# Optimization experiments

Hardware: AMD Instinct MI355X
Metric: run time of the kernel (lower is better)

## Reference

```python
import jax, jax.numpy as jnp
import numpy as np

B, T, C = 2, 2048, 1024
N_HEADS = 16
HEAD_DIM = C // N_HEADS

def setup_inputs() -> dict:
    key = jax.random.key(0)
    k1, k2, k3 = jax.random.split(key, 3)
    x = jax.random.normal(k1, (B, T, C), dtype=jnp.float32)
    W_qkv = jax.random.normal(k2, (C, 3 * C), dtype=jnp.float32) * (1.0 / np.sqrt(C))
    W_out = jax.random.normal(k3, (C, C), dtype=jnp.float32) * (1.0 / np.sqrt(C))
    return {"x": x, "W_qkv": W_qkv, "W_out": W_out}

def reference(x, W_qkv, W_out):
    b, t, c = x.shape
    qkv = jnp.einsum('btc,cd->btd', x, W_qkv)  # [B,T,3C]
    q, k, v = jnp.split(qkv, 3, axis=-1)
    # [B, H, T, hd]
    q = q.reshape(b, t, N_HEADS, HEAD_DIM).transpose(0, 2, 1, 3)
    k = k.reshape(b, t, N_HEADS, HEAD_DIM).transpose(0, 2, 1, 3)
    v = v.reshape(b, t, N_HEADS, HEAD_DIM).transpose(0, 2, 1, 3)
    scale = 1.0 / jnp.sqrt(jnp.asarray(HEAD_DIM, dtype=x.dtype))
    attn = jnp.einsum('bhqd,bhkd->bhqk', q, k) * scale  # [B,H,T,T]
    causal = jnp.tril(jnp.ones((t, t), dtype=bool))
    attn = jnp.where(causal, attn, jnp.asarray(-1e9, dtype=attn.dtype))
    attn = jax.nn.softmax(attn, axis=-1)
    out = jnp.einsum('bhqk,bhkd->bhqd', attn, v)
    out = out.transpose(0, 2, 1, 3).reshape(b, t, c)
    return jnp.einsum('btc,cd->btd', out, W_out)
```

## Files before the change

### kernel.cpp

```cpp
#include <hip/hip_runtime.h>
#include <hip/hip_bf16.h>

typedef __attribute__((ext_vector_type(8))) short short8;
typedef __attribute__((ext_vector_type(4))) short bf16x4;
typedef __attribute__((ext_vector_type(4))) float floatx4;

#define T_SEQ 2048
#define NH    16
#define HD    64
#define QSCALE 0.18033688f

#define MFMA16(a, b, c) __builtin_amdgcn_mfma_f32_16x16x16bf16_1k(a, b, c, 0, 0, 0)
#define MFMA32(a, b, c) __builtin_amdgcn_mfma_f32_16x16x32_bf16(a, b, c, 0, 0, 0)

__device__ __forceinline__ ushort f2bf(float f) {
    union { float f; unsigned u; } un; un.f = f;
    unsigned r = un.u + 0x7fff + ((un.u >> 16) & 1);
    return (ushort)(r >> 16);
}
__device__ __forceinline__ unsigned pkbf(float a, float b) {
    __hip_bfloat162 t = __float22bfloat162_rn(float2{a, b});
    return *reinterpret_cast<unsigned*>(&t);
}

typedef const __attribute__((address_space(1))) unsigned int* gp1_t;
typedef __attribute__((address_space(3))) unsigned int* lp3_t;
__device__ __forceinline__ void gl_lds16(const ushort* g, ushort* l) {
    __builtin_amdgcn_global_load_lds((gp1_t)g, (lp3_t)l, 16, 0, 0);
}

__global__ void prep_kernel(const float* __restrict__ Wqkv, const float* __restrict__ Wout,
                            const float* __restrict__ x, ushort* __restrict__ wt_qkv,
                            ushort* __restrict__ wt_out, ushort* __restrict__ x_bf) {
    __shared__ ushort tile[32][33];
    const int bid = blockIdx.x;
    if (bid >= 4096) {
        size_t i = ((size_t)(bid - 4096) * 256 + threadIdx.x) * 8;
        float4 f0 = *(const float4*)(x + i);
        float4 f1 = *(const float4*)(x + i + 4);
        short8 v;
        v[0] = (short)f2bf(f0.x); v[1] = (short)f2bf(f0.y);
        v[2] = (short)f2bf(f0.z); v[3] = (short)f2bf(f0.w);
        v[4] = (short)f2bf(f1.x); v[5] = (short)f2bf(f1.y);
        v[6] = (short)f2bf(f1.z); v[7] = (short)f2bf(f1.w);
        *(short8*)(x_bf + i) = v;
        return;
    }
    const float* in; ushort* out; int R, C, gx, gy;
    if (bid < 3072) { in = Wqkv; out = wt_qkv; R = 1024; C = 3072; gx = bid % 96; gy = bid / 96; }
    else            { int t = bid - 3072; in = Wout; out = wt_out; R = 1024; C = 1024; gx = t & 31; gy = t >> 5; }
    const int tx = threadIdx.x & 31, ty = threadIdx.x >> 5;
    const int bx = gx * 32, by = gy * 32;
    #pragma unroll
    for (int i = ty; i < 32; i += 8)
        tile[i][tx] = f2bf(in[(size_t)(by + i) * C + bx + tx]);
    __syncthreads();
    #pragma unroll
    for (int i = ty; i < 32; i += 8)
        out[(size_t)(bx + i) * R + by + tx] = tile[tx][i];
}

template <int EPI>
__global__ __launch_bounds__(256, 2)
void gemm_bt(const ushort* __restrict__ A, const ushort* __restrict__ Bt,
             void* __restrict__ O0, ushort* __restrict__ O1, ushort* __restrict__ O2,
             int M, int N, int K) {
    __shared__ __align__(16) ushort smem[8704];
    ushort* As = smem;
    ushort* Bs = smem + 4096;
    const int tid  = threadIdx.x;
    const int wave = tid >> 6, lane = tid & 63;
    const int quad = lane >> 4, l16 = lane & 15;
    const int wm = (wave >> 1) * 64, wn = (wave & 1) * 64;
    const int m0 = blockIdx.x * 128, n0 = blockIdx.y * 128;

    const int c0 = tid, c1 = tid + 256;
    const int row0 = c0 >> 2, row1 = c1 >> 2;
    const int g0 = (((c0 & 3) ^ ((row0 >> 1) & 3))) * 8;
    const int g1 = (((c1 & 3) ^ ((row1 >> 1) & 3))) * 8;
    const ushort* aP0 = A  + (size_t)(m0 + row0) * K + g0;
    const ushort* aP1 = A  + (size_t)(m0 + row1) * K + g1;
    const ushort* bP0 = Bt + (size_t)(n0 + row0) * K + g0;
    const ushort* bP1 = Bt + (size_t)(n0 + row1) * K + g1;

    floatx4 acc[4][4];
    #pragma unroll
    for (int i = 0; i < 4; i++)
        #pragma unroll
        for (int j = 0; j < 4; j++)
            acc[i][j] = (floatx4){0.f, 0.f, 0.f, 0.f};

    const int col_sw = (quad ^ ((l16 >> 1) & 3)) * 8;

    for (int k0 = 0; k0 < K; k0 += 32) {
        __syncthreads();
        gl_lds16(aP0 + k0, &As[c0 * 8]);
        gl_lds16(aP1 + k0, &As[c1 * 8]);
        gl_lds16(bP0 + k0, &Bs[c0 * 8]);
        gl_lds16(bP1 + k0, &Bs[c1 * 8]);
        __syncthreads();
        short8 af[4], bf[4];
        #pragma unroll
        for (int i = 0; i < 4; i++)
            af[i] = *(const short8*)(&As[(wm + i * 16 + l16) * 32 + col_sw]);
        #pragma unroll
        for (int j = 0; j < 4; j++)
            bf[j] = *(const short8*)(&Bs[(wn + j * 16 + l16) * 32 + col_sw]);
        #pragma unroll
        for (int i = 0; i < 4; i++)
            #pragma unroll
            for (int j = 0; j < 4; j++)
                acc[i][j] = __builtin_amdgcn_mfma_f32_16x16x32_bf16(af[i], bf[j], acc[i][j], 0, 0, 0);
    }

    if (EPI == 0 && n0 >= 2048) {
        const int b = m0 >> 11;
        const int t0 = m0 & 2047;
        const int head0 = (n0 - 2048) >> 6;
        __syncthreads();
        #pragma unroll
        for (int nh = 0; nh < 2; nh++) {
            if ((wave & 1) == nh) {
                #pragma unroll
                for (int j = 0; j < 4; j++)
                    #pragma unroll
                    for (int i = 0; i < 4; i++) {
                        int nl = j * 16 + l16;
                        int mB = wm + i * 16 + quad * 4;
                        *(unsigned*)(&smem[nl * 136 + mB])     = pkbf(acc[i][j][0], acc[i][j][1]);
                        *(unsigned*)(&smem[nl * 136 + mB + 2]) = pkbf(acc[i][j][2], acc[i][j][3]);
                    }
            }
            __syncthreads();
            #pragma unroll
            for (int cc = 0; cc < 4; cc++) {
                int c = cc * 256 + tid;
                int row = c >> 4, mcol = (c & 15) * 8;
                uint4 v = *(const uint4*)(&smem[row * 136 + mcol]);
                *(uint4*)(&O2[((size_t)(b * NH + head0 + nh) * HD + row) * T_SEQ + t0 + mcol]) = v;
            }
            __syncthreads();
        }
        return;
    }

    #pragma unroll
    for (int i = 0; i < 4; i++) {
        #pragma unroll
        for (int j = 0; j < 4; j++) {
            #pragma unroll
            for (int r = 0; r < 4; r++) {
                int m = m0 + wm + i * 16 + quad * 4 + r;
                int n = n0 + wn + j * 16 + l16;
                if (EPI == 0) {
                    int b = m >> 11, t = m & 2047;
                    int part = n >> 10, c = n & 1023;
                    int head = c >> 6, off = c & 63;
                    float av = acc[i][j][r];
                    if (part == 0) av *= QSCALE;
                    ushort v = f2bf(av);
                    if (part == 0) ((ushort*)O0)[(((size_t)(b * NH + head)) * T_SEQ + t) * HD + off] = v;
                    else           O1[(((size_t)(b * NH + head)) * T_SEQ + t) * HD + off] = v;
                } else {
                    ((float*)O0)[(size_t)m * N + n] = acc[i][j][r];
                }
            }
        }
    }
}

__device__ __forceinline__ void softmax_step(floatx4 s[4], float& mst, float& lst,
                                             floatx4 o[4], bf16x4 pf[4]) {
    float t0 = fmaxf(fmaxf(s[0][0], s[0][1]), fmaxf(s[0][2], s[0][3]));
    float t1 = fmaxf(fmaxf(s[1][0], s[1][1]), fmaxf(s[1][2], s[1][3]));
    float t2 = fmaxf(fmaxf(s[2][0], s[2][1]), fmaxf(s[2][2], s[2][3]));
    float t3 = fmaxf(fmaxf(s[3][0], s[3][1]), fmaxf(s[3][2], s[3][3]));
    float t = fmaxf(fmaxf(t0, t1), fmaxf(t2, t3));
    t = fmaxf(t, __shfl_xor(t, 16));
    t = fmaxf(t, __shfl_xor(t, 32));
    if (!__all(t - mst <= 8.0f)) {
        float mnew  = fmaxf(mst, t);
        float alpha = exp2f(mst - mnew);
        mst = mnew;
        lst *= alpha;
        #pragma unroll
        for (int db = 0; db < 4; db++)
            #pragma unroll
            for (int r = 0; r < 4; r++) o[db][r] *= alpha;
    }
    float lsum = 0.f;
    #pragma unroll
    for (int j = 0; j < 4; j++) {
        float p0 = exp2f(s[j][0] - mst);
        float p1 = exp2f(s[j][1] - mst);
        float p2 = exp2f(s[j][2] - mst);
        float p3 = exp2f(s[j][3] - mst);
        lsum += (p0 + p1) + (p2 + p3);
        union { bf16x4 v; unsigned u[2]; } pu;
        pu.u[0] = pkbf(p0, p1);
        pu.u[1] = pkbf(p2, p3);
        pf[j] = pu.v;
    }
    lsum += __shfl_xor(lsum, 16);
    lsum += __shfl_xor(lsum, 32);
    lst += lsum;
}

__global__ __launch_bounds__(256, 2)
void attn_kernel(const ushort* __restrict__ Q, const ushort* __restrict__ Kk,
                 const ushort* __restrict__ Vt, ushort* __restrict__ Oout) {
    __shared__ __align__(16) ushort Ks[2][64 * 64];
    __shared__ __align__(16) ushort Vs[2][64 * 64];
    const int tid  = threadIdx.x;
    const int wave = tid >> 6, lane = tid & 63;
    const int quad = lane >> 4, l16 = lane & 15;
    const int idx = blockIdx.x;
    const int bh = idx & 31;
    const int jp = idx >> 5;
    const int p  = (jp < 8) ? jp : (15 - (jp - 8));
    const int qtA = p, qtB = 31 - p;
    const int b = bh >> 4, h = bh & 15;

    const ushort* qp = Q  + (size_t)bh * T_SEQ * HD;
    const ushort* kp = Kk + (size_t)bh * T_SEQ * HD;
    const ushort* vp = Vt + (size_t)bh * HD * T_SEQ;

    const int q0A = qtA * 64 + wave * 16;
    const int q0B = qtB * 64 + wave * 16;

    short8 qfA[2], qfB[2];
    #pragma unroll
    for (int kb = 0; kb < 2; kb++) {
        qfA[kb] = *(const short8*)(qp + (size_t)(q0A + l16) * HD + kb * 32 + quad * 8);
        qfB[kb] = *(const short8*)(qp + (size_t)(q0B + l16) * HD + kb * 32 + quad * 8);
    }

    floatx4 oA[4], oB[4];
    #pragma unroll
    for (int db = 0; db < 4; db++) {
        oA[db] = (floatx4){0.f, 0.f, 0.f, 0.f};
        oB[db] = (floatx4){0.f, 0.f, 0.f, 0.f};
    }
    float mA = -1e30f, lA = 0.f, mB = -1e30f, lB = 0.f;

    const int c0 = tid, c1 = tid + 256;
    const int r0 = c0 >> 3, r1 = c1 >> 3;
    const int g0 = ((c0 & 7) ^ (r0 & 7)) * 8;
    const int g1 = ((c1 & 7) ^ (r1 & 7)) * 8;
    const size_t koff0 = (size_t)r0 * HD + g0,     koff1 = (size_t)r1 * HD + g1;
    const size_t voff0 = (size_t)r0 * T_SEQ + g0,  voff1 = (size_t)r1 * T_SEQ + g1;

    gl_lds16(kp + koff0, &Ks[0][c0 * 8]);
    gl_lds16(kp + koff1, &Ks[0][c1 * 8]);
    gl_lds16(vp + voff0, &Vs[0][c0 * 8]);
    gl_lds16(vp + voff1, &Vs[0][c1 * 8]);

    const int xsw = (l16 & 7), qh = quad >> 1, ql = quad & 1;
    const int ka0 = l16 * 64 + ((quad ^ xsw) * 8);
    const int ka1 = l16 * 64 + (((4 + quad) ^ xsw) * 8);
    int va[4];
    #pragma unroll
    for (int jj = 0; jj < 4; jj++)
        va[jj] = l16 * 64 + (((2 * jj + qh) ^ xsw) * 8) + ql * 4;

#define ATT_STEP(BUF, KT)                                                        \
    {                                                                            \
        __syncthreads();                                                         \
        if ((KT) < qtB) {                                                        \
            const size_t kbase = (size_t)((KT) + 1) * 64 * HD;                   \
            const int    vbase = ((KT) + 1) * 64;                                \
            gl_lds16(kp + kbase + koff0, &Ks[(BUF) ^ 1][c0 * 8]);                \
            gl_lds16(kp + kbase + koff1, &Ks[(BUF) ^ 1][c1 * 8]);                \
            gl_lds16(vp + vbase + voff0, &Vs[(BUF) ^ 1][c0 * 8]);                \
            gl_lds16(vp + vbase + voff1, &Vs[(BUF) ^ 1][c1 * 8]);                \
        }                                                                        \
        if ((KT) <= qtA) {                                                       \
                                \
            floatx4 sA[4], sB[4];                                                \
            _Pragma("unroll")                                                    \
            for (int jj = 0; jj < 4; jj++) {                                     \
                sA[jj] = (floatx4){0.f, 0.f, 0.f, 0.f};                          \
                sB[jj] = (floatx4){0.f, 0.f, 0.f, 0.f};                          \
            }                                                                    \
            __builtin_amdgcn_s_setprio(1);                                       \
            _Pragma("unroll")                                                    \
            for (int jj = 0; jj < 4; jj++) {                                     \
                short8 kf0 = *(const short8*)(&Ks[BUF][ka0 + jj * 1024]);        \
                sB[jj] = MFMA32(kf0, qfB[0], sB[jj]);                            \
                sA[jj] = MFMA32(kf0, qfA[0], sA[jj]);                            \
            }                                                                    \
            _Pragma("unroll")                                                    \
            for (int jj = 0; jj < 4; jj++) {                                     \
                short8 kf1 = *(const short8*)(&Ks[BUF][ka1 + jj * 1024]);        \
                sB[jj] = MFMA32(kf1, qfB[1], sB[jj]);                            \
                sA[jj] = MFMA32(kf1, qfA[1], sA[jj]);                            \
            }                                                                    \
            __builtin_amdgcn_s_setprio(0);                                       \
            if ((KT) == qtA) {                                                   \
                _Pragma("unroll")                                                \
                for (int jj = 0; jj < 4; jj++)                                   \
                    _Pragma("unroll")                                            \
                    for (int rr = 0; rr < 4; rr++)                               \
                        if (jj * 16 + quad * 4 + rr > wave * 16 + l16)           \
                            sA[jj][rr] = -1e30f;                                 \
            }                                                                    \
            bf16x4 pfA[4], pfB[4];                                               \
            softmax_step(sB, mB, lB, oB, pfB);                                   \
            softmax_step(sA, mA, lA, oA, pfA);                                   \
            __builtin_amdgcn_s_setprio(1);                                       \
            _Pragma("unroll")                                                    \
            for (int jj = 0; jj < 4; jj++)                                       \
                _Pragma("unroll")                                                \
                for (int db = 0; db < 4; db++) {                                 \
                    bf16x4 vf = *(const bf16x4*)(&Vs[BUF][va[jj] + db * 1024]);  \
                    oB[db] = MFMA16(vf, pfB[jj], oB[db]);                        \
                    oA[db] = MFMA16(vf, pfA[jj], oA[db]);                        \
                }                                                                \
            __builtin_amdgcn_s_setprio(0);                                       \
        } else {                                                                 \
                                                  \
            floatx4 sB[4];                                                       \
            _Pragma("unroll")                                                    \
            for (int jj = 0; jj < 4; jj++) sB[jj] = (floatx4){0.f, 0.f, 0.f, 0.f}; \
            __builtin_amdgcn_s_setprio(1);                                       \
            _Pragma("unroll")                                                    \
            for (int jj = 0; jj < 4; jj++) {                                     \
                short8 kf0 = *(const short8*)(&Ks[BUF][ka0 + jj * 1024]);        \
                sB[jj] = MFMA32(kf0, qfB[0], sB[jj]);                            \
            }                                                                    \
            _Pragma("unroll")                                                    \
            for (int jj = 0; jj < 4; jj++) {                                     \
                short8 kf1 = *(const short8*)(&Ks[BUF][ka1 + jj * 1024]);        \
                sB[jj] = MFMA32(kf1, qfB[1], sB[jj]);                            \
            }                                                                    \
            __builtin_amdgcn_s_setprio(0);                                       \
            if ((KT) == qtB) {                                                   \
                _Pragma("unroll")                                                \
                for (int jj = 0; jj < 4; jj++)                                   \
                    _Pragma("unroll")                                            \
                    for (int rr = 0; rr < 4; rr++)                               \
                        if (jj * 16 + quad * 4 + rr > wave * 16 + l16)           \
                            sB[jj][rr] = -1e30f;                                 \
            }                                                                    \
            bf16x4 pfB[4];                                                       \
            softmax_step(sB, mB, lB, oB, pfB);                                   \
            __builtin_amdgcn_s_setprio(1);                                       \
            _Pragma("unroll")                                                    \
            for (int jj = 0; jj < 4; jj++)                                       \
                _Pragma("unroll")                                                \
                for (int db = 0; db < 4; db++) {                                 \
                    bf16x4 vf = *(const bf16x4*)(&Vs[BUF][va[jj] + db * 1024]);  \
                    oB[db] = MFMA16(vf, pfB[jj], oB[db]);                        \
                }                                                                \
            __builtin_amdgcn_s_setprio(0);                                       \
        }                                                                        \
    }

    int kt = 0;
    for (; kt + 1 <= qtB; kt += 2) {
        ATT_STEP(0, kt)
        ATT_STEP(1, kt + 1)
    }
    if (kt <= qtB) ATT_STEP(0, kt)
#undef ATT_STEP

    {
        const float inv = 1.0f / lB;
        const int t = q0B + l16;
        #pragma unroll
        for (int db = 0; db < 4; db++) {
            union { ushort4 w; unsigned u[2]; } ou;
            ou.u[0] = pkbf(oB[db][0] * inv, oB[db][1] * inv);
            ou.u[1] = pkbf(oB[db][2] * inv, oB[db][3] * inv);
            *(ushort4*)(Oout + (((size_t)b * T_SEQ + t) * NH + h) * HD + db * 16 + quad * 4) = ou.w;
        }
    }
    {
        const float inv = 1.0f / lA;
        const int t = q0A + l16;
        #pragma unroll
        for (int db = 0; db < 4; db++) {
            union { ushort4 w; unsigned u[2]; } ou;
            ou.u[0] = pkbf(oA[db][0] * inv, oA[db][1] * inv);
            ou.u[1] = pkbf(oA[db][2] * inv, oA[db][3] * inv);
            *(ushort4*)(Oout + (((size_t)b * T_SEQ + t) * NH + h) * HD + db * 16 + quad * 4) = ou.w;
        }
    }
}

extern "C" void kernel_launch(void* const* d_in, const int* in_sizes, int n_in,
                              void* d_out, int out_size, void* d_ws, size_t ws_size,
                              hipStream_t stream) {
    const float* x    = (const float*)d_in[0];
    const float* Wqkv = (const float*)d_in[1];
    const float* Wout = (const float*)d_in[2];
    ushort* ws = (ushort*)d_ws;

    ushort* wt_qkv = ws;
    ushort* wt_out = wt_qkv + 3072 * 1024;
    ushort* q_ws   = wt_out + 1024 * 1024;
    ushort* k_ws   = q_ws + 4194304;
    ushort* v_t    = k_ws + 4194304;
    ushort* a_out  = v_t + 4194304;
    ushort* x_bf   = a_out + 4194304;

    prep_kernel<<<dim3(6144), 256, 0, stream>>>(Wqkv, Wout, x, wt_qkv, wt_out, x_bf);

    gemm_bt<0><<<dim3(32, 24), 256, 0, stream>>>(x_bf, wt_qkv, q_ws, k_ws, v_t, 4096, 3072, 1024);

    attn_kernel<<<dim3(512), 256, 0, stream>>>(q_ws, k_ws, v_t, a_out);

    gemm_bt<1><<<dim3(32, 8), 256, 0, stream>>>(a_out, wt_out, (float*)d_out, nullptr, nullptr,
                                                4096, 1024, 1024);
}
```

Baseline: 185.5 us.

## Stage 128-key K/V tiles per barrier and defer softmax row-sum reductions

The attention loop now stages 128 keys of K and V per double-buffered LDS stage and processes them as two 64-key sub-steps. This halves the number of __syncthreads barriers and global-to-LDS staging rounds per block. The softmax keeps per-lane partial row sums, cross-lane reducing them only once in the epilogue, and does the row-max shuffles only when a rescale is needed. In exchange, LDS use per block doubles to 64KB, which could limit occupancy, and the last tile may load keys that are never used.

New measurement: 180.0 us. 1.03x faster.

```diff
diff --git a/kernel.cpp b/kernel.cpp
--- a/kernel.cpp
+++ b/kernel.cpp
@@ -169,48 +169,44 @@
     }
 }
 
-__device__ __forceinline__ void softmax_step(floatx4 s[4], float& mst, float& lst,
+__device__ __forceinline__ void softmax_step(floatx4 s[4], float& mst, float& ll,
                                              floatx4 o[4], bf16x4 pf[4]) {
     float t0 = fmaxf(fmaxf(s[0][0], s[0][1]), fmaxf(s[0][2], s[0][3]));
     float t1 = fmaxf(fmaxf(s[1][0], s[1][1]), fmaxf(s[1][2], s[1][3]));
     float t2 = fmaxf(fmaxf(s[2][0], s[2][1]), fmaxf(s[2][2], s[2][3]));
     float t3 = fmaxf(fmaxf(s[3][0], s[3][1]), fmaxf(s[3][2], s[3][3]));
-    float t = fmaxf(fmaxf(t0, t1), fmaxf(t2, t3));
-    t = fmaxf(t, __shfl_xor(t, 16));
-    t = fmaxf(t, __shfl_xor(t, 32));
+    float t  = fmaxf(fmaxf(t0, t1), fmaxf(t2, t3));
     if (!__all(t - mst <= 8.0f)) {
+        t = fmaxf(t, __shfl_xor(t, 16));
+        t = fmaxf(t, __shfl_xor(t, 32));
         float mnew  = fmaxf(mst, t);
         float alpha = exp2f(mst - mnew);
         mst = mnew;
-        lst *= alpha;
+        ll  *= alpha;
         #pragma unroll
         for (int db = 0; db < 4; db++)
             #pragma unroll
             for (int r = 0; r < 4; r++) o[db][r] *= alpha;
     }
-    float lsum = 0.f;
     #pragma unroll
     for (int j = 0; j < 4; j++) {
         float p0 = exp2f(s[j][0] - mst);
         float p1 = exp2f(s[j][1] - mst);
         float p2 = exp2f(s[j][2] - mst);
         float p3 = exp2f(s[j][3] - mst);
-        lsum += (p0 + p1) + (p2 + p3);
+        ll += (p0 + p1) + (p2 + p3);
         union { bf16x4 v; unsigned u[2]; } pu;
         pu.u[0] = pkbf(p0, p1);
         pu.u[1] = pkbf(p2, p3);
         pf[j] = pu.v;
     }
-    lsum += __shfl_xor(lsum, 16);
-    lsum += __shfl_xor(lsum, 32);
-    lst += lsum;
 }
 
 __global__ __launch_bounds__(256, 2)
 void attn_kernel(const ushort* __restrict__ Q, const ushort* __restrict__ Kk,
                  const ushort* __restrict__ Vt, ushort* __restrict__ Oout) {
-    __shared__ __align__(16) ushort Ks[2][64 * 64];
-    __shared__ __align__(16) ushort Vs[2][64 * 64];
+    __shared__ __align__(16) ushort Ks[2][128 * 64];
+    __shared__ __align__(16) ushort Vs[2][64 * 128];
     const int tid  = threadIdx.x;
     const int wave = tid >> 6, lane = tid & 63;
     const int quad = lane >> 4, l16 = lane & 15;
@@ -241,19 +237,31 @@
         oA[db] = (floatx4){0.f, 0.f, 0.f, 0.f};
         oB[db] = (floatx4){0.f, 0.f, 0.f, 0.f};
     }
-    float mA = -1e30f, lA = 0.f, mB = -1e30f, lB = 0.f;
-
-    const int c0 = tid, c1 = tid + 256;
-    const int r0 = c0 >> 3, r1 = c1 >> 3;
-    const int g0 = ((c0 & 7) ^ (r0 & 7)) * 8;
-    const int g1 = ((c1 & 7) ^ (r1 & 7)) * 8;
-    const size_t koff0 = (size_t)r0 * HD + g0,     koff1 = (size_t)r1 * HD + g1;
-    const size_t voff0 = (size_t)r0 * T_SEQ + g0,  voff1 = (size_t)r1 * T_SEQ + g1;
-
-    gl_lds16(kp + koff0, &Ks[0][c0 * 8]);
-    gl_lds16(kp + koff1, &Ks[0][c1 * 8]);
-    gl_lds16(vp + voff0, &Vs[0][c0 * 8]);
-    gl_lds16(vp + voff1, &Vs[0][c1 * 8]);
+    float mA = -1e30f, llA = 0.f, mB = -1e30f, llB = 0.f;
+
+    int koff[4], voff[4];
+    #pragma unroll
+    for (int j = 0; j < 4; j++) {
+        int c = tid + j * 256;
+        int kr = c >> 3;
+        koff[j] = kr * HD + (((c & 7) ^ (kr & 7)) * 8);
+        int vr = c >> 4;
+        voff[j] = vr * T_SEQ + ((((c & 15) ^ (vr & 7))) * 8);
+    }
+
+#define STAGE(BUF, I)                                                            \
+    {                                                                            \
+        const ushort* kg = kp + (size_t)(I) * 128 * HD;                          \
+        const ushort* vg = vp + (I) * 128;                                       \
+        gl_lds16(kg + koff[0], &Ks[BUF][(tid      ) * 8]);                       \
+        gl_lds16(kg + koff[1], &Ks[BUF][(tid + 256) * 8]);                       \
+        gl_lds16(kg + koff[2], &Ks[BUF][(tid + 512) * 8]);                       \
+        gl_lds16(kg + koff[3], &Ks[BUF][(tid + 768) * 8]);                       \
+        gl_lds16(vg + voff[0], &Vs[BUF][(tid      ) * 8]);                       \
+        gl_lds16(vg + voff[1], &Vs[BUF][(tid + 256) * 8]);                       \
+        gl_lds16(vg + voff[2], &Vs[BUF][(tid + 512) * 8]);                       \
+        gl_lds16(vg + voff[3], &Vs[BUF][(tid + 768) * 8]);                       \
+    }
 
     const int xsw = (l16 & 7), qh = quad >> 1, ql = quad & 1;
     const int ka0 = l16 * 64 + ((quad ^ xsw) * 8);
@@ -261,21 +269,12 @@
     int va[4];
     #pragma unroll
     for (int jj = 0; jj < 4; jj++)
-        va[jj] = l16 * 64 + (((2 * jj + qh) ^ xsw) * 8) + ql * 4;
-
-#define ATT_STEP(BUF, KT)                                                        \
+        va[jj] = l16 * 128 + (((2 * jj + qh) ^ xsw) * 8) + ql * 4;
+
+#define SUBCOMP(BUF, ST, KT)                                                     \
     {                                                                            \
-        __syncthreads();                                                         \
-        if ((KT) < qtB) {                                                        \
-            const size_t kbase = (size_t)((KT) + 1) * 64 * HD;                   \
-            const int    vbase = ((KT) + 1) * 64;                                \
-            gl_lds16(kp + kbase + koff0, &Ks[(BUF) ^ 1][c0 * 8]);                \
-            gl_lds16(kp + kbase + koff1, &Ks[(BUF) ^ 1][c1 * 8]);                \
-            gl_lds16(vp + vbase + voff0, &Vs[(BUF) ^ 1][c0 * 8]);                \
-            gl_lds16(vp + vbase + voff1, &Vs[(BUF) ^ 1][c1 * 8]);                \
-        }                                                                        \
-        if ((KT) <= qtA) {                                                       \
-                                \
+        const int kt_ = (KT);                                                    \
+        if (kt_ <= qtA) {                                                        \
             floatx4 sA[4], sB[4];                                                \
             _Pragma("unroll")                                                    \
             for (int jj = 0; jj < 4; jj++) {                                     \
@@ -285,18 +284,18 @@
             __builtin_amdgcn_s_setprio(1);                                       \
             _Pragma("unroll")                                                    \
             for (int jj = 0; jj < 4; jj++) {                                     \
-                short8 kf0 = *(const short8*)(&Ks[BUF][ka0 + jj * 1024]);        \
+                short8 kf0 = *(const short8*)(&Ks[BUF][(ST) * 4096 + jj * 1024 + ka0]); \
                 sB[jj] = MFMA32(kf0, qfB[0], sB[jj]);                            \
                 sA[jj] = MFMA32(kf0, qfA[0], sA[jj]);                            \
             }                                                                    \
             _Pragma("unroll")                                                    \
             for (int jj = 0; jj < 4; jj++) {                                     \
-                short8 kf1 = *(const short8*)(&Ks[BUF][ka1 + jj * 1024]);        \
+                short8 kf1 = *(const short8*)(&Ks[BUF][(ST) * 4096 + jj * 1024 + ka1]); \
                 sB[jj] = MFMA32(kf1, qfB[1], sB[jj]);                            \
                 sA[jj] = MFMA32(kf1, qfA[1], sA[jj]);                            \
             }                                                                    \
             __builtin_amdgcn_s_setprio(0);                                       \
-            if ((KT) == qtA) {                                                   \
+            if (kt_ == qtA) {                                                    \
                 _Pragma("unroll")                                                \
                 for (int jj = 0; jj < 4; jj++)                                   \
                     _Pragma("unroll")                                            \
@@ -305,36 +304,35 @@
                             sA[jj][rr] = -1e30f;                                 \
             }                                                                    \
             bf16x4 pfA[4], pfB[4];                                               \
-            softmax_step(sB, mB, lB, oB, pfB);                                   \
-            softmax_step(sA, mA, lA, oA, pfA);                                   \
+            softmax_step(sB, mB, llB, oB, pfB);                                  \
+            softmax_step(sA, mA, llA, oA, pfA);                                  \
             __builtin_amdgcn_s_setprio(1);                                       \
             _Pragma("unroll")                                                    \
             for (int jj = 0; jj < 4; jj++)                                       \
                 _Pragma("unroll")                                                \
                 for (int db = 0; db < 4; db++) {                                 \
-                    bf16x4 vf = *(const bf16x4*)(&Vs[BUF][va[jj] + db * 1024]);  \
+                    bf16x4 vf = *(const bf16x4*)(&Vs[BUF][va[jj] + (ST) * 64 + db * 2048]); \
                     oB[db] = MFMA16(vf, pfB[jj], oB[db]);                        \
                     oA[db] = MFMA16(vf, pfA[jj], oA[db]);                        \
                 }                                                                \
             __builtin_amdgcn_s_setprio(0);                                       \
         } else {                                                                 \
-                                                  \
             floatx4 sB[4];                                                       \
             _Pragma("unroll")                                                    \
             for (int jj = 0; jj < 4; jj++) sB[jj] = (floatx4){0.f, 0.f, 0.f, 0.f}; \
             __builtin_amdgcn_s_setprio(1);                                       \
             _Pragma("unroll")                                                    \
             for (int jj = 0; jj < 4; jj++) {                                     \
-                short8 kf0 = *(const short8*)(&Ks[BUF][ka0 + jj * 1024]);        \
+                short8 kf0 = *(const short8*)(&Ks[BUF][(ST) * 4096 + jj * 1024 + ka0]); \
                 sB[jj] = MFMA32(kf0, qfB[0], sB[jj]);                            \
             }                                                                    \
             _Pragma("unroll")                                                    \
             for (int jj = 0; jj < 4; jj++) {                                     \
-                short8 kf1 = *(const short8*)(&Ks[BUF][ka1 + jj * 1024]);        \
+                short8 kf1 = *(const short8*)(&Ks[BUF][(ST) * 4096 + jj * 1024 + ka1]); \
                 sB[jj] = MFMA32(kf1, qfB[1], sB[jj]);                            \
             }                                                                    \
             __builtin_amdgcn_s_setprio(0);                                       \
-            if ((KT) == qtB) {                                                   \
+            if (kt_ == qtB) {                                                    \
                 _Pragma("unroll")                                                \
                 for (int jj = 0; jj < 4; jj++)                                   \
                     _Pragma("unroll")                                            \
@@ -343,28 +341,47 @@
                             sB[jj][rr] = -1e30f;                                 \
             }                                                                    \
             bf16x4 pfB[4];                                                       \
-            softmax_step(sB, mB, lB, oB, pfB);                                   \
+            softmax_step(sB, mB, llB, oB, pfB);                                  \
             __builtin_amdgcn_s_setprio(1);                                       \
             _Pragma("unroll")                                                    \
             for (int jj = 0; jj < 4; jj++)                                       \
                 _Pragma("unroll")                                                \
                 for (int db = 0; db < 4; db++) {                                 \
-                    bf16x4 vf = *(const bf16x4*)(&Vs[BUF][va[jj] + db * 1024]);  \
+                    bf16x4 vf = *(const bf16x4*)(&Vs[BUF][va[jj] + (ST) * 64 + db * 2048]); \
                     oB[db] = MFMA16(vf, pfB[jj], oB[db]);                        \
                 }                                                                \
             __builtin_amdgcn_s_setprio(0);                                       \
         }                                                                        \
     }
 
-    int kt = 0;
-    for (; kt + 1 <= qtB; kt += 2) {
-        ATT_STEP(0, kt)
-        ATT_STEP(1, kt + 1)
-    }
-    if (kt <= qtB) ATT_STEP(0, kt)
-#undef ATT_STEP
+#define ITER(BUF, I)                                                             \
+    {                                                                            \
+        __syncthreads();                                                         \
+        if ((I) + 1 < NT) STAGE((BUF) ^ 1, (I) + 1)                              \
+        SUBCOMP(BUF, 0, 2 * (I))                                                 \
+        {                                                                        \
+            const int kt1 = 2 * (I) + 1;                                         \
+            if (kt1 <= qtB) SUBCOMP(BUF, 1, kt1)                                 \
+        }                                                                        \
+    }
+
+    const int NT = (qtB + 2) >> 1;
+    STAGE(0, 0)
+
+    int i = 0;
+    for (; i + 1 < NT; i += 2) {
+        ITER(0, i)
+        ITER(1, i + 1)
+    }
+    if (i < NT) ITER(0, i)
+#undef ITER
+#undef SUBCOMP
+#undef STAGE
 
     {
+        float lB = llB;
+        lB += __shfl_xor(lB, 16);
+        lB += __shfl_xor(lB, 32);
         const float inv = 1.0f / lB;
         const int t = q0B + l16;
         #pragma unroll
@@ -376,6 +393,9 @@
         }
     }
     {
+        float lA = llA;
+        lA += __shfl_xor(lA, 16);
+        lA += __shfl_xor(lA, 32);
         const float inv = 1.0f / lA;
         const int t = q0A + l16;
         #pragma unroll
```
